# Kernel tuning notes

Hardware: AMD Instinct MI355X
Metric: run time of the kernel (lower is better)

The kernel has to match this reference:

```python
import jax, jax.numpy as jnp
import numpy as np

POS_SIZE = 63
LATENT_SIZE = 256
NUM_CLUSTERS = 64
N = 524288


def setup_inputs() -> dict:
    key = jax.random.key(0)
    k1, k2, k3, k4 = jax.random.split(key, 4)
    X = jax.random.normal(k1, (N, POS_SIZE + LATENT_SIZE), dtype=jnp.float32)
    cluster_ids = jax.random.randint(k2, (N,), 0, NUM_CLUSTERS, dtype=jnp.int32)
    # nn.Linear weights have shape [out_features, in_features]
    W_pos = jax.random.normal(k3, (3 * NUM_CLUSTERS, POS_SIZE), dtype=jnp.float32) * 0.1
    W_feat = jax.random.normal(k4, (3 * NUM_CLUSTERS, LATENT_SIZE), dtype=jnp.float32) * 0.1
    return {"X": X, "cluster_ids": cluster_ids, "W_pos": W_pos, "W_feat": W_feat}


def reference(X, cluster_ids, W_pos, W_feat):
    # Dense projections: [N, 3*num_clusters]
    rgb_clusters = (
        jnp.einsum("np,cp->nc", X[:, :POS_SIZE], W_pos)
        + jnp.einsum("nl,cl->nc", X[:, POS_SIZE:], W_feat)
    )
    # Per-row gather of the 3 columns belonging to this row's cluster.
    cols = 3 * cluster_ids[:, None] + jnp.arange(3, dtype=cluster_ids.dtype)[None, :]  # [N, 3]
    rgb = jnp.take_along_axis(rgb_clusters, cols, axis=1)  # [N, 3]
    return rgb
```

## Files before the change

### kernel.cpp

```cpp
#include <hip/hip_runtime.h>


constexpr int POS = 63;
constexpr int LAT = 256;
constexpr int DIM = 319;
constexpr int NCH = 192;
constexpr int PW_DWORDS = NCH * 192;
constexpr size_t PW_BYTES = (size_t)PW_DWORDS * 4;

__device__ __forceinline__ unsigned f2bf(float f) {
    unsigned u = __float_as_uint(f);
    return (u + 0x7fffu + ((u >> 16) & 1u)) >> 16;
}

__global__ __launch_bounds__(256) void pack_weights(
    const float* __restrict__ Wp,
    const float* __restrict__ Wf,
    unsigned* __restrict__ pw)
{
    const int idx = blockIdx.x * 256 + threadIdx.x;
    if (idx >= PW_DWORDS) return;
    const int ch  = idx / 192;
    const int rem = idx - ch * 192;
    const int d   = rem >> 6;
    const int l   = rem & 63;
    const int klo = l + 128 * d;
    const int khi = klo + 64;
    auto wat = [&](int k) -> float {
        if (k < POS) return Wp[ch * POS + k];
        if (k < DIM) return Wf[ch * LAT + (k - POS)];
        return 0.f;
    };
    pw[idx] = f2bf(wat(klo)) | (f2bf(wat(khi)) << 16);
}

template <int CTRL>
__device__ __forceinline__ float dpp_add_step(float x) {
    int s = __builtin_amdgcn_update_dpp(0, __float_as_int(x), CTRL,
                                        0xF, 0xF, true);
    return x + __int_as_float(s);
}
__device__ __forceinline__ float wave_reduce_sum(float x) {
    x = dpp_add_step<0x111>(x);
    x = dpp_add_step<0x112>(x);
    x = dpp_add_step<0x114>(x);
    x = dpp_add_step<0x118>(x);
    x = dpp_add_step<0x142>(x);
    x = dpp_add_step<0x143>(x);
    return x;
}

__device__ __forceinline__ float blo(unsigned w) { return __uint_as_float(w << 16); }
__device__ __forceinline__ float bhi(unsigned w) { return __uint_as_float(w & 0xffff0000u); }

__global__ __launch_bounds__(256) void lad_seq(
    const float* __restrict__ X,
    const int*   __restrict__ cid,
    const unsigned* __restrict__ pw,
    float*       __restrict__ out,
    int n)
{
    const int l    = threadIdx.x & 63;
    const int wave = (int)((blockIdx.x * blockDim.x + threadIdx.x) >> 6);
    if (wave >= n) return;

    const size_t row = (size_t)wave;
    const float* xr = X + row * (size_t)DIM;
    const int c3 = 3 * __builtin_amdgcn_readfirstlane(cid[row]);
    const unsigned* wb = pw + (size_t)c3 * 192;

    const float x0 = xr[l];
    const float x1 = xr[l + 64];
    const float x2 = xr[l + 128];
    const float x3 = xr[l + 192];
    const float x4 = (l < 63) ? xr[l + 256] : 0.f;

    const unsigned wA0 = wb[l],       wA1 = wb[64 + l],  wA2 = wb[128 + l];
    const unsigned wB0 = wb[192 + l], wB1 = wb[256 + l], wB2 = wb[320 + l];
    const unsigned wC0 = wb[384 + l], wC1 = wb[448 + l], wC2 = wb[512 + l];

    float a0 = x0 * blo(wA0);
    a0 = fmaf(x1, bhi(wA0), a0);
    a0 = fmaf(x2, blo(wA1), a0);
    a0 = fmaf(x3, bhi(wA1), a0);
    a0 = fmaf(x4, blo(wA2), a0);

    float a1 = x0 * blo(wB0);
    a1 = fmaf(x1, bhi(wB0), a1);
    a1 = fmaf(x2, blo(wB1), a1);
    a1 = fmaf(x3, bhi(wB1), a1);
    a1 = fmaf(x4, blo(wB2), a1);

    float a2 = x0 * blo(wC0);
    a2 = fmaf(x1, bhi(wC0), a2);
    a2 = fmaf(x2, blo(wC1), a2);
    a2 = fmaf(x3, bhi(wC1), a2);
    a2 = fmaf(x4, blo(wC2), a2);

    a0 = wave_reduce_sum(a0);
    a1 = wave_reduce_sum(a1);
    a2 = wave_reduce_sum(a2);

    if (l == 63) {
        float* o = out + row * 3;
        o[0] = a0; o[1] = a1; o[2] = a2;
    }
}

__global__ __launch_bounds__(256) void lad_fallback(
    const float* __restrict__ X,
    const int*   __restrict__ cid,
    const float* __restrict__ Wp,
    const float* __restrict__ Wf,
    float*       __restrict__ out,
    int n)
{
    const int lane = threadIdx.x & 63;
    const int wave = (int)((blockIdx.x * blockDim.x + threadIdx.x) >> 6);
    if (wave >= n) return;
    const size_t row = (size_t)wave;
    const float* xrow = X + row * (size_t)DIM;
    const float* xf   = xrow + POS;
    const int c3 = cid[row] * 3;
    const float* wp0 = Wp + (size_t)c3 * POS;
    const float* wf0 = Wf + (size_t)c3 * LAT;
    float a0 = 0.f, a1 = 0.f, a2 = 0.f;
#pragma unroll
    for (int i = 0; i < 4; ++i) {
        const int k = lane + 64 * i;
        const float x = xf[k];
        a0 = fmaf(x, wf0[k], a0);
        a1 = fmaf(x, wf0[k + LAT], a1);
        a2 = fmaf(x, wf0[k + 2 * LAT], a2);
    }
    if (lane < POS) {
        const float x = xrow[lane];
        a0 = fmaf(x, wp0[lane], a0);
        a1 = fmaf(x, wp0[lane + POS], a1);
        a2 = fmaf(x, wp0[lane + 2 * POS], a2);
    }
    a0 = wave_reduce_sum(a0);
    a1 = wave_reduce_sum(a1);
    a2 = wave_reduce_sum(a2);
    if (lane == 63) {
        float* o = out + row * 3;
        o[0] = a0; o[1] = a1; o[2] = a2;
    }
}

extern "C" void kernel_launch(void* const* d_in, const int* in_sizes, int n_in,
                              void* d_out, int out_size, void* d_ws, size_t ws_size,
                              hipStream_t stream) {
    const float* X   = (const float*)d_in[0];
    const int*   cid = (const int*)d_in[1];
    const float* Wp  = (const float*)d_in[2];
    const float* Wf  = (const float*)d_in[3];
    float* out = (float*)d_out;
    const int n = in_sizes[1];

    if (ws_size >= PW_BYTES) {
        unsigned* pw = (unsigned*)d_ws;
        pack_weights<<<(PW_DWORDS + 255) / 256, 256, 0, stream>>>(Wp, Wf, pw);
        const int blocks = (n + 3) / 4;
        lad_seq<<<blocks, 256, 0, stream>>>(X, cid, pw, out, n);
    } else {
        const int blocks = (n + 3) / 4;
        lad_fallback<<<blocks, 256, 0, stream>>>(X, cid, Wp, Wf, out, n);
    }
}
```

Baseline: 174.0 us.

## Use persistent grid-stride waves with software-pipelined prefetch of next row

```diff
diff --git a/kernel.cpp b/kernel.cpp
--- a/kernel.cpp
+++ b/kernel.cpp
@@ -7,6 +7,8 @@
 constexpr int NCH = 192;
 constexpr int PW_DWORDS = NCH * 192;
 constexpr size_t PW_BYTES = (size_t)PW_DWORDS * 4;
+constexpr int NBLK = 2048;
+constexpr int NWAVES = NBLK * 4;
 
 __device__ __forceinline__ unsigned f2bf(float f) {
     unsigned u = __float_as_uint(f);
@@ -53,57 +55,89 @@
 __device__ __forceinline__ float blo(unsigned w) { return __uint_as_float(w << 16); }
 __device__ __forceinline__ float bhi(unsigned w) { return __uint_as_float(w & 0xffff0000u); }
 
-__global__ __launch_bounds__(256) void lad_seq(
+__global__ __launch_bounds__(256, 8) void lad_seq32(
     const float* __restrict__ X,
     const int*   __restrict__ cid,
     const unsigned* __restrict__ pw,
     float*       __restrict__ out,
     int n)
 {
-    const int l    = threadIdx.x & 63;
-    const int wave = (int)((blockIdx.x * blockDim.x + threadIdx.x) >> 6);
-    if (wave >= n) return;
-
-    const size_t row = (size_t)wave;
-    const float* xr = X + row * (size_t)DIM;
-    const int c3 = 3 * __builtin_amdgcn_readfirstlane(cid[row]);
-    const unsigned* wb = pw + (size_t)c3 * 192;
-
-    const float x0 = xr[l];
-    const float x1 = xr[l + 64];
-    const float x2 = xr[l + 128];
-    const float x3 = xr[l + 192];
-    const float x4 = (l < 63) ? xr[l + 256] : 0.f;
-
-    const unsigned wA0 = wb[l],       wA1 = wb[64 + l],  wA2 = wb[128 + l];
-    const unsigned wB0 = wb[192 + l], wB1 = wb[256 + l], wB2 = wb[320 + l];
-    const unsigned wC0 = wb[384 + l], wC1 = wb[448 + l], wC2 = wb[512 + l];
-
-    float a0 = x0 * blo(wA0);
-    a0 = fmaf(x1, bhi(wA0), a0);
-    a0 = fmaf(x2, blo(wA1), a0);
-    a0 = fmaf(x3, bhi(wA1), a0);
-    a0 = fmaf(x4, blo(wA2), a0);
-
-    float a1 = x0 * blo(wB0);
-    a1 = fmaf(x1, bhi(wB0), a1);
-    a1 = fmaf(x2, blo(wB1), a1);
-    a1 = fmaf(x3, bhi(wB1), a1);
-    a1 = fmaf(x4, blo(wB2), a1);
-
-    float a2 = x0 * blo(wC0);
-    a2 = fmaf(x1, bhi(wC0), a2);
-    a2 = fmaf(x2, blo(wC1), a2);
-    a2 = fmaf(x3, bhi(wC1), a2);
-    a2 = fmaf(x4, blo(wC2), a2);
-
-    a0 = wave_reduce_sum(a0);
-    a1 = wave_reduce_sum(a1);
-    a2 = wave_reduce_sum(a2);
-
-    if (l == 63) {
-        float* o = out + row * 3;
-        o[0] = a0; o[1] = a1; o[2] = a2;
+    const int l  = threadIdx.x & 63;
+    int r = blockIdx.x * 4 + (threadIdx.x >> 6);
+    if (r >= n) return;
+
+    int c_cur = 3 * __builtin_amdgcn_readfirstlane(cid[r]);
+    const float* xr = X + (size_t)r * DIM;
+    float xa0 = xr[l];
+    float xa1 = xr[l + 64];
+    float xa2 = xr[l + 128];
+    float xa3 = xr[l + 192];
+    float xa4 = (l < 63) ? xr[l + 256] : 0.f;
+
+    const unsigned* wb = pw + (size_t)c_cur * 192;
+    unsigned wA0 = wb[l],       wA1 = wb[64 + l],  wA2 = wb[128 + l];
+    unsigned wB0 = wb[192 + l], wB1 = wb[256 + l], wB2 = wb[320 + l];
+    unsigned wC0 = wb[384 + l], wC1 = wb[448 + l], wC2 = wb[512 + l];
+
+    int rn = r + NWAVES;
+    int c_nxt = (rn < n) ? 3 * __builtin_amdgcn_readfirstlane(cid[rn]) : 0;
+
+    while (true) {
+        const bool has = (rn < n);
+
+        float xb0 = 0.f, xb1 = 0.f, xb2 = 0.f, xb3 = 0.f, xb4 = 0.f;
+        unsigned nA0 = 0, nA1 = 0, nA2 = 0, nB0 = 0, nB1 = 0, nB2 = 0,
+                 nC0 = 0, nC1 = 0, nC2 = 0;
+        int c_nn = 0;
+        if (has) {
+            const float* xn = X + (size_t)rn * DIM;
+            xb0 = xn[l];
+            xb1 = xn[l + 64];
+            xb2 = xn[l + 128];
+            xb3 = xn[l + 192];
+            if (l < 63) xb4 = xn[l + 256];
+            const unsigned* wn = pw + (size_t)c_nxt * 192;
+            nA0 = wn[l];       nA1 = wn[64 + l];  nA2 = wn[128 + l];
+            nB0 = wn[192 + l]; nB1 = wn[256 + l]; nB2 = wn[320 + l];
+            nC0 = wn[384 + l]; nC1 = wn[448 + l]; nC2 = wn[512 + l];
+            if (rn + NWAVES < n)
+                c_nn = 3 * __builtin_amdgcn_readfirstlane(cid[rn + NWAVES]);
+        }
+
+        float a0 = xa0 * blo(wA0);
+        a0 = fmaf(xa1, bhi(wA0), a0);
+        a0 = fmaf(xa2, blo(wA1), a0);
+        a0 = fmaf(xa3, bhi(wA1), a0);
+        a0 = fmaf(xa4, blo(wA2), a0);
+
+        float a1 = xa0 * blo(wB0);
+        a1 = fmaf(xa1, bhi(wB0), a1);
+        a1 = fmaf(xa2, blo(wB1), a1);
+        a1 = fmaf(xa3, bhi(wB1), a1);
+        a1 = fmaf(xa4, blo(wB2), a1);
+
+        float a2 = xa0 * blo(wC0);
+        a2 = fmaf(xa1, bhi(wC0), a2);
+        a2 = fmaf(xa2, blo(wC1), a2);
+        a2 = fmaf(xa3, bhi(wC1), a2);
+        a2 = fmaf(xa4, blo(wC2), a2);
+
+        a0 = wave_reduce_sum(a0);
+        a1 = wave_reduce_sum(a1);
+        a2 = wave_reduce_sum(a2);
+
+        if (l == 63) {
+            float* o = out + (size_t)r * 3;
+            o[0] = a0; o[1] = a1; o[2] = a2;
+        }
+
+        if (!has) break;
+        r = rn; rn += NWAVES;
+        c_cur = c_nxt; c_nxt = c_nn;
+        xa0 = xb0; xa1 = xb1; xa2 = xb2; xa3 = xb3; xa4 = xb4;
+        wA0 = nA0; wA1 = nA1; wA2 = nA2;
+        wB0 = nB0; wB1 = nB1; wB2 = nB2;
+        wC0 = nC0; wC1 = nC1; wC2 = nC2;
     }
 }
 
@@ -161,8 +195,7 @@
     if (ws_size >= PW_BYTES) {
         unsigned* pw = (unsigned*)d_ws;
         pack_weights<<<(PW_DWORDS + 255) / 256, 256, 0, stream>>>(Wp, Wf, pw);
-        const int blocks = (n + 3) / 4;
-        lad_seq<<<blocks, 256, 0, stream>>>(X, cid, pw, out, n);
+        lad_seq32<<<NBLK, 256, 0, stream>>>(X, cid, pw, out, n);
     } else {
         const int blocks = (n + 3) / 4;
         lad_fallback<<<blocks, 256, 0, stream>>>(X, cid, Wp, Wf, out, n);
```

Result: slower. 191.1 us (+9.8%).
